# Kernel tuning notes

Measured on AMD Instinct MI355X. Metric: run time of the kernel, lower is better.

## Reference

```python
import jax, jax.numpy as jnp
import numpy as np

DIM = 768
NUM_HEADS = 12
HEAD_DIM = DIM // NUM_HEADS
SCALE = HEAD_DIM ** -0.5


def setup_inputs() -> dict:
    key = jax.random.key(0)
    k1, k2, k3, k4, k5 = jax.random.split(key, 5)
    B, N, C = 4, 2048, DIM
    x = jax.random.normal(k1, (B, N, C), dtype=jnp.float32)
    xpos = jax.random.randint(k2, (B, N), 0, 2048, dtype=jnp.int32)
    # torch Linear weights: qkv (no bias), proj (with bias)
    lim_qkv = (1.0 / C) ** 0.5
    w_qkv = jax.random.uniform(k3, (3 * C, C), minval=-lim_qkv, maxval=lim_qkv, dtype=jnp.float32)
    w_proj = jax.random.uniform(k4, (C, C), minval=-lim_qkv, maxval=lim_qkv, dtype=jnp.float32)
    b_proj = jax.random.uniform(k5, (C,), minval=-lim_qkv, maxval=lim_qkv, dtype=jnp.float32)
    return {"x": x, "xpos": xpos, "w_qkv": w_qkv, "w_proj": w_proj, "b_proj": b_proj}


def reference(x, xpos, w_qkv, w_proj, b_proj):
    B, N, C = x.shape
    H, Dh = NUM_HEADS, HEAD_DIM
    # fused QKV projection: [B,N,3C] -> [B,N,3,H,Dh] -> [B,H,3,N,Dh]
    qkv = (x @ w_qkv.T).reshape(B, N, 3, H, Dh).transpose(0, 3, 2, 1, 4)
    q, k, v = qkv[:, :, 0], qkv[:, :, 1], qkv[:, :, 2]
    # rope is None -> xpos unused
    # naive attention: materialize full [B,H,N,N] scores (matches pytorch_naive)
    scores = jnp.einsum('bhqd,bhkd->bhqk', q, k) * SCALE
    attn = jax.nn.softmax(scores, axis=-1)
    out = jnp.einsum('bhqk,bhkd->bhqd', attn, v)  # [B,H,N,Dh]
    out = out.transpose(0, 2, 1, 3).reshape(B, N, C)
    return out @ w_proj.T + b_proj
```

## Files before the change

### kernel.cpp

```cpp
#include <hip/hip_runtime.h>
#include <math.h>

typedef __bf16 bf16;
typedef __attribute__((ext_vector_type(4))) __bf16 bf16x4;
typedef __attribute__((ext_vector_type(8))) __bf16 bf16x8;
typedef __attribute__((ext_vector_type(4))) float f32x4;
typedef __attribute__((ext_vector_type(4))) unsigned int u32x4;

#define AS1 __attribute__((address_space(1)))
#define AS3 __attribute__((address_space(3)))

__device__ __forceinline__ void gload16(const void* g, void* l) {
  __builtin_amdgcn_global_load_lds((const AS1 void*)g, (AS3 void*)l, 16, 0, 0);
}

__device__ __forceinline__ unsigned int pack2bf(float lo, float hi) {
  union { unsigned int u; __bf16 h[2]; } w;
  w.h[0] = (bf16)lo; w.h[1] = (bf16)hi;
  return w.u;
}

#define DIM 768
#define NH  12
#define HD  64
#define B_  4
#define N_  2048
#define M_  (B_*N_)
#define BH_ (B_*NH)

__global__ void convert_all(const float4* __restrict__ x,
                            const float4* __restrict__ wq,
                            const float4* __restrict__ wp,
                            bf16x4* __restrict__ xb,
                            bf16x4* __restrict__ wqb,
                            bf16x4* __restrict__ wpb) {
  const int nx = M_*DIM/4, nq = 3*DIM*DIM/4, np = DIM*DIM/4;
  const int total = nx + nq + np;
  for (int i = blockIdx.x*blockDim.x + threadIdx.x; i < total;
       i += gridDim.x*blockDim.x) {
    float4 v; bf16x4* dst;
    if (i < nx)           { v = x[i];         dst = xb  + i;         }
    else if (i < nx + nq) { v = wq[i-nx];     dst = wqb + (i-nx);    }
    else                  { v = wp[i-nx-nq];  dst = wpb + (i-nx-nq); }
    bf16x4 o = { (bf16)v.x, (bf16)v.y, (bf16)v.z, (bf16)v.w };
    *dst = o;
  }
}

template<int EPI>
__global__ __launch_bounds__(256)
void gemm_bt(const bf16* __restrict__ A, const bf16* __restrict__ B,
             bf16* __restrict__ qv, bf16* __restrict__ kv_, bf16* __restrict__ vt,
             const float* __restrict__ bprj, float* __restrict__ out) {
  constexpr int K = DIM;
  __shared__ __align__(16) bf16 As[128*32];
  __shared__ __align__(16) bf16 Bs[128*32];
  const int tid = threadIdx.x;
  const int wave = tid >> 6, lane = tid & 63;
  const int l15 = lane & 15, lg = lane >> 4;
  const int wr = wave >> 1, wc = wave & 1;
  const int m0 = blockIdx.y * 128, n0 = blockIdx.x * 128;

  f32x4 acc[4][4] = {};
  const int pbase = wave*2048 + lane*16;

  for (int kb = 0; kb < K; kb += 32) {
    __syncthreads();
#pragma unroll
    for (int i = 0; i < 2; i++) {
      int p = pbase + i*1024;
      int row = p >> 6, cb = p & 63;
      gload16((const char*)A + ((size_t)(m0+row)*K + kb)*2 + cb, (char*)As + p);
      gload16((const char*)B + ((size_t)(n0+row)*K + kb)*2 + cb, (char*)Bs + p);
    }
    __syncthreads();
    bf16x8 af[4], bfr[4];
#pragma unroll
    for (int f = 0; f < 4; f++) {
      af[f]  = *(const bf16x8*)(As + (wr*64 + f*16 + l15)*32 + lg*8);
      bfr[f] = *(const bf16x8*)(Bs + (wc*64 + f*16 + l15)*32 + lg*8);
    }
#pragma unroll
    for (int fm = 0; fm < 4; fm++)
#pragma unroll
      for (int fn = 0; fn < 4; fn++)
        acc[fm][fn] = __builtin_amdgcn_mfma_f32_16x16x32_bf16(af[fm], bfr[fn],
                                                              acc[fm][fn], 0, 0, 0);
  }

  if (EPI == 0) {
    const int c0 = n0 + wc*64;
    const int t = c0 / DIM;
    const int hcol = (c0 % DIM) >> 6;
#pragma unroll
    for (int fm = 0; fm < 4; fm++) {
      const int gm0 = m0 + wr*64 + fm*16 + (lg<<2);
      const int b = gm0 >> 11, nn0 = gm0 & 2047;
      const size_t bh = (size_t)b*NH + hcol;
#pragma unroll
      for (int fn = 0; fn < 4; fn++) {
        const int d = fn*16 + l15;
        if (t == 0) {
#pragma unroll
          for (int r = 0; r < 4; r++)
            qv[(bh*N_ + nn0 + r)*HD + d] = (bf16)(acc[fm][fn][r] * 0.125f);
        } else if (t == 1) {
#pragma unroll
          for (int r = 0; r < 4; r++)
            kv_[(bh*N_ + nn0 + r)*HD + d] = (bf16)acc[fm][fn][r];
        } else {
          bf16x4 pk = { (bf16)acc[fm][fn][0], (bf16)acc[fm][fn][1],
                        (bf16)acc[fm][fn][2], (bf16)acc[fm][fn][3] };
          *(bf16x4*)(vt + (bh*HD + d)*N_ + nn0) = pk;
        }
      }
    }
  } else {
#pragma unroll
    for (int fn = 0; fn < 4; fn++) {
      const int c = n0 + wc*64 + fn*16 + l15;
      const float bias = bprj[c];
#pragma unroll
      for (int fm = 0; fm < 4; fm++) {
        const int gm0 = m0 + wr*64 + fm*16 + (lg<<2);
#pragma unroll
        for (int r = 0; r < 4; r++)
          out[(size_t)(gm0 + r)*DIM + c] = acc[fm][fn][r] + bias;
      }
    }
  }
}

__global__ __launch_bounds__(256)
void attn_fwd(const bf16* __restrict__ Q, const bf16* __restrict__ Kb,
              const bf16* __restrict__ Vt, bf16* __restrict__ AO) {
  __shared__ __align__(16) bf16 Ks[2][64*64];
  __shared__ __align__(16) bf16 Vs[2][64*64];
  const int tid = threadIdx.x;
  const int wave = tid >> 6, lane = tid & 63;
  const int l15 = lane & 15, lg = lane >> 4;
  const int bh = blockIdx.y;
  const int b = bh / NH, h = bh % NH;
  const int q0 = blockIdx.x*128 + wave*32;

  const bf16* Qbase = Q + (size_t)bh*N_*HD;
  bf16x8 qf[2][2];
#pragma unroll
  for (int fq = 0; fq < 2; fq++)
#pragma unroll
    for (int ks = 0; ks < 2; ks++)
      qf[fq][ks] = *(const bf16x8*)(Qbase + (size_t)(q0 + fq*16 + l15)*HD + ks*32 + lg*8);

  f32x4 Ot[2][4] = {};
  float m_[2] = { -INFINITY, -INFINITY };
  float l_[2] = { 0.f, 0.f };

  const char* Kg = (const char*)(Kb + (size_t)bh*N_*HD);
  const char* Vg = (const char*)(Vt + (size_t)bh*HD*N_);
  const int pbase = wave*2048 + lane*16;
  const bool lower = (lane < 32);
  const bool q03 = (lg == 0) || (lg == 3);

#define STAGE(buf, kv)                                                      \
  {                                                                         \
    _Pragma("unroll")                                                       \
    for (int i = 0; i < 2; i++) {                                           \
      int p = pbase + i*1024;                                               \
      int r = p >> 7, cbp = p & 127;                                        \
      int cb = cbp ^ ((r & 7) << 4);                                        \
      gload16(Kg + (size_t)((kv) + r)*128 + cb, (char*)Ks[buf] + p);        \
      gload16(Vg + (size_t)r*(N_*2) + (kv)*2 + cb, (char*)Vs[buf] + p);     \
    }                                                                       \
  }

  STAGE(0, 0);

  for (int t = 0; t < N_/64; ++t) {
    __syncthreads();
    if (t + 1 < N_/64) STAGE((t+1)&1, (t+1)*64);
    const char* Kc = (const char*)Ks[t&1];
    const char* Vc = (const char*)Vs[t&1];

    f32x4 s[2][4] = {};
#pragma unroll
    for (int ks = 0; ks < 2; ks++) {
      bf16x8 kf[4];
#pragma unroll
      for (int fk = 0; fk < 4; fk++) {
        int r = fk*16 + l15;
        int cb = (ks*64 + lg*16) ^ ((r & 7) << 4);
        kf[fk] = *(const bf16x8*)(Kc + r*128 + cb);
      }
#pragma unroll
      for (int fq = 0; fq < 2; fq++)
#pragma unroll
        for (int fk = 0; fk < 4; fk++)
          s[fq][fk] = __builtin_amdgcn_mfma_f32_16x16x32_bf16(kf[fk], qf[fq][ks],
                                                              s[fq][fk], 0, 0, 0);
    }

    unsigned int paw[2][2][4];
#pragma unroll
    for (int fq = 0; fq < 2; fq++) {
      float mx = s[fq][0][0];
#pragma unroll
      for (int fk = 0; fk < 4; fk++)
#pragma unroll
        for (int r = 0; r < 4; r++) mx = fmaxf(mx, s[fq][fk][r]);
      mx = fmaxf(mx, __shfl_xor(mx, 16));
      mx = fmaxf(mx, __shfl_xor(mx, 32));
      if (!__all(mx - m_[fq] <= 6.0f)) {
        float mn = fmaxf(m_[fq], mx);
        float c = __expf(m_[fq] - mn);
        m_[fq] = mn; l_[fq] *= c;
#pragma unroll
        for (int fd = 0; fd < 4; fd++) Ot[fq][fd] *= c;
      }
      float pe[4][4]; float rs = 0.f;
#pragma unroll
      for (int fk = 0; fk < 4; fk++)
#pragma unroll
        for (int r = 0; r < 4; r++) {
          pe[fk][r] = __expf(s[fq][fk][r] - m_[fq]);
          rs += pe[fk][r];
        }
      rs += __shfl_xor(rs, 16);
      rs += __shfl_xor(rs, 32);
      l_[fq] += rs;

      unsigned int pk[4][2];
#pragma unroll
      for (int fk = 0; fk < 4; fk++)
#pragma unroll
        for (int rp = 0; rp < 2; rp++)
          pk[fk][rp] = pack2bf(pe[fk][2*rp], pe[fk][2*rp+1]);

      unsigned int Eo[2][2], Er[2][2], rB[2][2];
#pragma unroll
      for (int fh = 0; fh < 2; fh++)
#pragma unroll
        for (int rp = 0; rp < 2; rp++) {
          unsigned int vA = lower ? pk[2*fh+1][rp] : pk[2*fh][rp];
          Er[fh][rp] = __shfl_xor((int)vA, 32);
          Eo[fh][rp] = lower ? pk[2*fh][rp] : pk[2*fh+1][rp];
        }
#pragma unroll
      for (int fh = 0; fh < 2; fh++)
#pragma unroll
        for (int rp = 0; rp < 2; rp++) {
          unsigned int vB = q03 ? Er[fh][rp] : Eo[fh][rp];
          rB[fh][rp] = __shfl_xor((int)vB, 16);
        }
#pragma unroll
      for (int ks = 0; ks < 2; ks++) {
#pragma unroll
        for (int rp = 0; rp < 2; rp++) {
          paw[fq][ks][rp] = (lg == 0) ? Eo[ks][rp] :
                            (lg == 1) ? rB[ks][rp] :
                            (lg == 2) ? Er[ks][rp] : rB[ks][rp];
          paw[fq][ks][2+rp] = (lg == 0) ? rB[ks][rp] :
                              (lg == 1) ? Er[ks][rp] :
                              (lg == 2) ? rB[ks][rp] : Eo[ks][rp];
        }
      }
    }

#pragma unroll
    for (int ks = 0; ks < 2; ks++) {
      bf16x8 vb[4];
#pragma unroll
      for (int fd = 0; fd < 4; fd++) {
        int r = fd*16 + l15;
        int cb = (ks*64 + lg*16) ^ ((r & 7) << 4);
        vb[fd] = *(const bf16x8*)(Vc + r*128 + cb);
      }
#pragma unroll
      for (int fq = 0; fq < 2; fq++) {
        u32x4 tw = { paw[fq][ks][0], paw[fq][ks][1], paw[fq][ks][2], paw[fq][ks][3] };
        bf16x8 pa = __builtin_bit_cast(bf16x8, tw);
#pragma unroll
        for (int fd = 0; fd < 4; fd++)
          Ot[fq][fd] = __builtin_amdgcn_mfma_f32_16x16x32_bf16(vb[fd], pa,
                                                               Ot[fq][fd], 0, 0, 0);
      }
    }
  }

#pragma unroll
  for (int fq = 0; fq < 2; fq++) {
    const float inv = 1.f / l_[fq];
    const int qrow = q0 + fq*16 + l15;
#pragma unroll
    for (int fd = 0; fd < 4; fd++) {
      bf16x4 pk4 = { (bf16)(Ot[fq][fd][0]*inv), (bf16)(Ot[fq][fd][1]*inv),
                     (bf16)(Ot[fq][fd][2]*inv), (bf16)(Ot[fq][fd][3]*inv) };
      *(bf16x4*)(AO + ((size_t)b*N_ + qrow)*DIM + h*HD + fd*16 + lg*4) = pk4;
    }
  }
#undef STAGE
}

extern "C" void kernel_launch(void* const* d_in, const int* in_sizes, int n_in,
                              void* d_out, int out_size, void* d_ws, size_t ws_size,
                              hipStream_t stream) {
  const float* x     = (const float*)d_in[0];
  const float* wqkv  = (const float*)d_in[2];
  const float* wproj = (const float*)d_in[3];
  const float* bproj = (const float*)d_in[4];
  float* out = (float*)d_out;

  char* ws = (char*)d_ws;
  bf16* xb    = (bf16*)ws;  ws += (size_t)M_*DIM*2;
  bf16* wqkvb = (bf16*)ws;  ws += (size_t)3*DIM*DIM*2;
  bf16* wprojb= (bf16*)ws;  ws += (size_t)DIM*DIM*2;
  bf16* qb    = (bf16*)ws;  ws += (size_t)BH_*N_*HD*2;
  bf16* kb    = (bf16*)ws;  ws += (size_t)BH_*N_*HD*2;
  bf16* vtb   = (bf16*)ws;  ws += (size_t)BH_*HD*N_*2;
  bf16* aob   = (bf16*)ws;  ws += (size_t)M_*DIM*2;

  convert_all<<<dim3(2048), dim3(256), 0, stream>>>(
      (const float4*)x, (const float4*)wqkv, (const float4*)wproj,
      (bf16x4*)xb, (bf16x4*)wqkvb, (bf16x4*)wprojb);

  gemm_bt<0><<<dim3(3*DIM/128, M_/128), dim3(256), 0, stream>>>(
      xb, wqkvb, qb, kb, vtb, nullptr, nullptr);

  attn_fwd<<<dim3(N_/128, BH_), dim3(256), 0, stream>>>(qb, kb, vtb, aob);

  gemm_bt<1><<<dim3(DIM/128, M_/128), dim3(256), 0, stream>>>(
      aob, wprojb, nullptr, nullptr, nullptr, bproj, out);
}
```

Measured before the change: 267.2 us.

## Halve attention query tile per block and switch softmax to exp2 with folded log2e

Each attention block now handles 64 queries (16 per wave) instead of 128, doubling the grid so more blocks are available to fill the GPU, at the cost of loading each K/V tile twice as often per query. The Q scale now folds in log2(e) so the softmax can use exp2f instead of __expf. The lazy-rescale threshold is raised to 8 in log2 units, and the row max uses a tree reduction. Per-wave MFMA work per K/V tile halves, which lowers register pressure but reduces the reuse of each shared-memory load.

```diff
diff --git a/kernel.cpp b/kernel.cpp
--- a/kernel.cpp
+++ b/kernel.cpp
@@ -27,6 +27,8 @@
 #define N_  2048
 #define M_  (B_*N_)
 #define BH_ (B_*NH)
+
+#define QSCALE 0.1803368801111244f
 
 __global__ void convert_all(const float4* __restrict__ x,
                             const float4* __restrict__ wq,
@@ -103,7 +105,7 @@
         if (t == 0) {
 #pragma unroll
           for (int r = 0; r < 4; r++)
-            qv[(bh*N_ + nn0 + r)*HD + d] = (bf16)(acc[fm][fn][r] * 0.125f);
+            qv[(bh*N_ + nn0 + r)*HD + d] = (bf16)(acc[fm][fn][r] * QSCALE);
         } else if (t == 1) {
 #pragma unroll
           for (int r = 0; r < 4; r++)
@@ -141,19 +143,16 @@
   const int l15 = lane & 15, lg = lane >> 4;
   const int bh = blockIdx.y;
   const int b = bh / NH, h = bh % NH;
-  const int q0 = blockIdx.x*128 + wave*32;
+  const int q0 = blockIdx.x*64 + wave*16;
 
   const bf16* Qbase = Q + (size_t)bh*N_*HD;
-  bf16x8 qf[2][2];
-#pragma unroll
-  for (int fq = 0; fq < 2; fq++)
-#pragma unroll
-    for (int ks = 0; ks < 2; ks++)
-      qf[fq][ks] = *(const bf16x8*)(Qbase + (size_t)(q0 + fq*16 + l15)*HD + ks*32 + lg*8);
-
-  f32x4 Ot[2][4] = {};
-  float m_[2] = { -INFINITY, -INFINITY };
-  float l_[2] = { 0.f, 0.f };
+  bf16x8 qf[2];
+#pragma unroll
+  for (int ks = 0; ks < 2; ks++)
+    qf[ks] = *(const bf16x8*)(Qbase + (size_t)(q0 + l15)*HD + ks*32 + lg*8);
+
+  f32x4 Ot[4] = {};
+  float m_ = -INFINITY, l_ = 0.f;
 
   const char* Kg = (const char*)(Kb + (size_t)bh*N_*HD);
   const char* Vg = (const char*)(Vt + (size_t)bh*HD*N_);
@@ -181,7 +180,7 @@
     const char* Kc = (const char*)Ks[t&1];
     const char* Vc = (const char*)Vs[t&1];
 
-    f32x4 s[2][4] = {};
+    f32x4 s[4] = {};
 #pragma unroll
     for (int ks = 0; ks < 2; ks++) {
       bf16x8 kf[4];
@@ -192,78 +191,75 @@
         kf[fk] = *(const bf16x8*)(Kc + r*128 + cb);
       }
 #pragma unroll
-      for (int fq = 0; fq < 2; fq++)
-#pragma unroll
-        for (int fk = 0; fk < 4; fk++)
-          s[fq][fk] = __builtin_amdgcn_mfma_f32_16x16x32_bf16(kf[fk], qf[fq][ks],
-                                                              s[fq][fk], 0, 0, 0);
-    }
-
-    unsigned int paw[2][2][4];
-#pragma unroll
-    for (int fq = 0; fq < 2; fq++) {
-      float mx = s[fq][0][0];
-#pragma unroll
       for (int fk = 0; fk < 4; fk++)
-#pragma unroll
-        for (int r = 0; r < 4; r++) mx = fmaxf(mx, s[fq][fk][r]);
-      mx = fmaxf(mx, __shfl_xor(mx, 16));
-      mx = fmaxf(mx, __shfl_xor(mx, 32));
-      if (!__all(mx - m_[fq] <= 6.0f)) {
-        float mn = fmaxf(m_[fq], mx);
-        float c = __expf(m_[fq] - mn);
-        m_[fq] = mn; l_[fq] *= c;
-#pragma unroll
-        for (int fd = 0; fd < 4; fd++) Ot[fq][fd] *= c;
-      }
-      float pe[4][4]; float rs = 0.f;
-#pragma unroll
-      for (int fk = 0; fk < 4; fk++)
-#pragma unroll
-        for (int r = 0; r < 4; r++) {
-          pe[fk][r] = __expf(s[fq][fk][r] - m_[fq]);
-          rs += pe[fk][r];
-        }
-      rs += __shfl_xor(rs, 16);
-      rs += __shfl_xor(rs, 32);
-      l_[fq] += rs;
-
-      unsigned int pk[4][2];
-#pragma unroll
-      for (int fk = 0; fk < 4; fk++)
-#pragma unroll
-        for (int rp = 0; rp < 2; rp++)
-          pk[fk][rp] = pack2bf(pe[fk][2*rp], pe[fk][2*rp+1]);
-
-      unsigned int Eo[2][2], Er[2][2], rB[2][2];
-#pragma unroll
-      for (int fh = 0; fh < 2; fh++)
-#pragma unroll
-        for (int rp = 0; rp < 2; rp++) {
-          unsigned int vA = lower ? pk[2*fh+1][rp] : pk[2*fh][rp];
-          Er[fh][rp] = __shfl_xor((int)vA, 32);
-          Eo[fh][rp] = lower ? pk[2*fh][rp] : pk[2*fh+1][rp];
-        }
-#pragma unroll
-      for (int fh = 0; fh < 2; fh++)
-#pragma unroll
-        for (int rp = 0; rp < 2; rp++) {
-          unsigned int vB = q03 ? Er[fh][rp] : Eo[fh][rp];
-          rB[fh][rp] = __shfl_xor((int)vB, 16);
-        }
-#pragma unroll
-      for (int ks = 0; ks < 2; ks++) {
-#pragma unroll
-        for (int rp = 0; rp < 2; rp++) {
-          paw[fq][ks][rp] = (lg == 0) ? Eo[ks][rp] :
-                            (lg == 1) ? rB[ks][rp] :
-                            (lg == 2) ? Er[ks][rp] : rB[ks][rp];
-          paw[fq][ks][2+rp] = (lg == 0) ? rB[ks][rp] :
-                              (lg == 1) ? Er[ks][rp] :
-                              (lg == 2) ? rB[ks][rp] : Eo[ks][rp];
-        }
-      }
-    }
+        s[fk] = __builtin_amdgcn_mfma_f32_16x16x32_bf16(kf[fk], qf[ks],
+                                                        s[fk], 0, 0, 0);
+    }
+
+    f32x4 m01, m23, m4;
+#pragma unroll
+    for (int r = 0; r < 4; r++) {
+      m01[r] = fmaxf(s[0][r], s[1][r]);
+      m23[r] = fmaxf(s[2][r], s[3][r]);
+      m4[r]  = fmaxf(m01[r], m23[r]);
+    }
+    float mx = fmaxf(fmaxf(m4[0], m4[1]), fmaxf(m4[2], m4[3]));
+    mx = fmaxf(mx, __shfl_xor(mx, 16));
+    mx = fmaxf(mx, __shfl_xor(mx, 32));
+    if (!__all(mx - m_ <= 8.0f)) {
+      float mn = fmaxf(m_, mx);
+      float c = exp2f(m_ - mn);
+      m_ = mn; l_ *= c;
+#pragma unroll
+      for (int fd = 0; fd < 4; fd++) Ot[fd] *= c;
+    }
+    float pe[4][4]; float rs = 0.f;
+#pragma unroll
+    for (int fk = 0; fk < 4; fk++)
+#pragma unroll
+      for (int r = 0; r < 4; r++) {
+        pe[fk][r] = exp2f(s[fk][r] - m_);
+        rs += pe[fk][r];
+      }
+    rs += __shfl_xor(rs, 16);
+    rs += __shfl_xor(rs, 32);
+    l_ += rs;
+
+    unsigned int pk[4][2];
+#pragma unroll
+    for (int fk = 0; fk < 4; fk++)
+#pragma unroll
+      for (int rp = 0; rp < 2; rp++)
+        pk[fk][rp] = pack2bf(pe[fk][2*rp], pe[fk][2*rp+1]);
+
+    unsigned int Eo[2][2], Er[2][2], rB[2][2];
+#pragma unroll
+    for (int fh = 0; fh < 2; fh++)
+#pragma unroll
+      for (int rp = 0; rp < 2; rp++) {
+        unsigned int vA = lower ? pk[2*fh+1][rp] : pk[2*fh][rp];
+        Er[fh][rp] = __shfl_xor((int)vA, 32);
+        Eo[fh][rp] = lower ? pk[2*fh][rp] : pk[2*fh+1][rp];
+      }
+#pragma unroll
+    for (int fh = 0; fh < 2; fh++)
+#pragma unroll
+      for (int rp = 0; rp < 2; rp++) {
+        unsigned int vB = q03 ? Er[fh][rp] : Eo[fh][rp];
+        rB[fh][rp] = __shfl_xor((int)vB, 16);
+      }
+    unsigned int paw[2][4];
+#pragma unroll
+    for (int ks = 0; ks < 2; ks++)
+#pragma unroll
+      for (int rp = 0; rp < 2; rp++) {
+        paw[ks][rp]   = (lg == 0) ? Eo[ks][rp] :
+                        (lg == 1) ? rB[ks][rp] :
+                        (lg == 2) ? Er[ks][rp] : rB[ks][rp];
+        paw[ks][2+rp] = (lg == 0) ? rB[ks][rp] :
+                        (lg == 1) ? Er[ks][rp] :
+                        (lg == 2) ? rB[ks][rp] : Eo[ks][rp];
+      }
 
 #pragma unroll
     for (int ks = 0; ks < 2; ks++) {
@@ -274,28 +270,22 @@
         int cb = (ks*64 + lg*16) ^ ((r & 7) << 4);
         vb[fd] = *(const bf16x8*)(Vc + r*128 + cb);
       }
-#pragma unroll
-      for (int fq = 0; fq < 2; fq++) {
-        u32x4 tw = { paw[fq][ks][0], paw[fq][ks][1], paw[fq][ks][2], paw[fq][ks][3] };
-        bf16x8 pa = __builtin_bit_cast(bf16x8, tw);
-#pragma unroll
-        for (int fd = 0; fd < 4; fd++)
-          Ot[fq][fd] = __builtin_amdgcn_mfma_f32_16x16x32_bf16(vb[fd], pa,
-                                                               Ot[fq][fd], 0, 0, 0);
-      }
-    }
-  }
-
-#pragma unroll
-  for (int fq = 0; fq < 2; fq++) {
-    const float inv = 1.f / l_[fq];
-    const int qrow = q0 + fq*16 + l15;
-#pragma unroll
-    for (int fd = 0; fd < 4; fd++) {
-      bf16x4 pk4 = { (bf16)(Ot[fq][fd][0]*inv), (bf16)(Ot[fq][fd][1]*inv),
-                     (bf16)(Ot[fq][fd][2]*inv), (bf16)(Ot[fq][fd][3]*inv) };
-      *(bf16x4*)(AO + ((size_t)b*N_ + qrow)*DIM + h*HD + fd*16 + lg*4) = pk4;
-    }
+      u32x4 tw = { paw[ks][0], paw[ks][1], paw[ks][2], paw[ks][3] };
+      bf16x8 pa = __builtin_bit_cast(bf16x8, tw);
+#pragma unroll
+      for (int fd = 0; fd < 4; fd++)
+        Ot[fd] = __builtin_amdgcn_mfma_f32_16x16x32_bf16(vb[fd], pa,
+                                                         Ot[fd], 0, 0, 0);
+    }
+  }
+
+  const float inv = 1.f / l_;
+  const int qrow = q0 + l15;
+#pragma unroll
+  for (int fd = 0; fd < 4; fd++) {
+    bf16x4 pk4 = { (bf16)(Ot[fd][0]*inv), (bf16)(Ot[fd][1]*inv),
+                   (bf16)(Ot[fd][2]*inv), (bf16)(Ot[fd][3]*inv) };
+    *(bf16x4*)(AO + ((size_t)b*N_ + qrow)*DIM + h*HD + fd*16 + lg*4) = pk4;
   }
 #undef STAGE
 }
@@ -325,7 +315,7 @@
   gemm_bt<0><<<dim3(3*DIM/128, M_/128), dim3(256), 0, stream>>>(
       xb, wqkvb, qb, kb, vtb, nullptr, nullptr);
 
-  attn_fwd<<<dim3(N_/128, BH_), dim3(256), 0, stream>>>(qb, kb, vtb, aob);
+  attn_fwd<<<dim3(N_/64, BH_), dim3(256), 0, stream>>>(qb, kb, vtb, aob);
 
   gemm_bt<1><<<dim3(DIM/128, M_/128), dim3(256), 0, stream>>>(
       aob, wprojb, nullptr, nullptr, nullptr, bproj, out);
```

Measured after the change: 294.6 us. +10.3%, slower.

## Split attention KV range across two blocks with a separate combine kernel

Applied to the files above, without the earlier changes.

Splits each attention block's key/value range into two halves on a third grid dimension. Each half writes unnormalised fp32 partial outputs plus running max and sum, and a new combine kernel merges them into the bf16 attention output. The Q scale now folds in log2(e), so the softmax can use exp2f; the rescale threshold is raised and the max reduction becomes a tree. This adds parallelism and shortens each block's loop, at the cost of extra fp32 partial traffic and an additional kernel launch.

```diff
diff --git a/kernel.cpp b/kernel.cpp
--- a/kernel.cpp
+++ b/kernel.cpp
@@ -27,6 +27,10 @@
 #define N_  2048
 #define M_  (B_*N_)
 #define BH_ (B_*NH)
+#define NSPLIT 2
+#define KVLEN (N_/NSPLIT)
+
+#define QSCALE 0.1803368801111244f
 
 __global__ void convert_all(const float4* __restrict__ x,
                             const float4* __restrict__ wq,
@@ -103,7 +107,7 @@
         if (t == 0) {
 #pragma unroll
           for (int r = 0; r < 4; r++)
-            qv[(bh*N_ + nn0 + r)*HD + d] = (bf16)(acc[fm][fn][r] * 0.125f);
+            qv[(bh*N_ + nn0 + r)*HD + d] = (bf16)(acc[fm][fn][r] * QSCALE);
         } else if (t == 1) {
 #pragma unroll
           for (int r = 0; r < 4; r++)
@@ -133,14 +137,15 @@
 
 __global__ __launch_bounds__(256)
 void attn_fwd(const bf16* __restrict__ Q, const bf16* __restrict__ Kb,
-              const bf16* __restrict__ Vt, bf16* __restrict__ AO) {
+              const bf16* __restrict__ Vt,
+              float* __restrict__ Opart, float* __restrict__ Mlpart) {
   __shared__ __align__(16) bf16 Ks[2][64*64];
   __shared__ __align__(16) bf16 Vs[2][64*64];
   const int tid = threadIdx.x;
   const int wave = tid >> 6, lane = tid & 63;
   const int l15 = lane & 15, lg = lane >> 4;
   const int bh = blockIdx.y;
-  const int b = bh / NH, h = bh % NH;
+  const int spl = blockIdx.z;
   const int q0 = blockIdx.x*128 + wave*32;
 
   const bf16* Qbase = Q + (size_t)bh*N_*HD;
@@ -155,8 +160,8 @@
   float m_[2] = { -INFINITY, -INFINITY };
   float l_[2] = { 0.f, 0.f };
 
-  const char* Kg = (const char*)(Kb + (size_t)bh*N_*HD);
-  const char* Vg = (const char*)(Vt + (size_t)bh*HD*N_);
+  const char* Kg = (const char*)(Kb + (size_t)bh*N_*HD) + (size_t)spl*KVLEN*128;
+  const char* Vg = (const char*)(Vt + (size_t)bh*HD*N_) + (size_t)spl*KVLEN*2;
   const int pbase = wave*2048 + lane*16;
   const bool lower = (lane < 32);
   const bool q03 = (lg == 0) || (lg == 3);
@@ -175,9 +180,9 @@
 
   STAGE(0, 0);
 
-  for (int t = 0; t < N_/64; ++t) {
+  for (int t = 0; t < KVLEN/64; ++t) {
     __syncthreads();
-    if (t + 1 < N_/64) STAGE((t+1)&1, (t+1)*64);
+    if (t + 1 < KVLEN/64) STAGE((t+1)&1, (t+1)*64);
     const char* Kc = (const char*)Ks[t&1];
     const char* Vc = (const char*)Vs[t&1];
 
@@ -202,16 +207,19 @@
     unsigned int paw[2][2][4];
 #pragma unroll
     for (int fq = 0; fq < 2; fq++) {
-      float mx = s[fq][0][0];
-#pragma unroll
-      for (int fk = 0; fk < 4; fk++)
-#pragma unroll
-        for (int r = 0; r < 4; r++) mx = fmaxf(mx, s[fq][fk][r]);
+      float mx = fmaxf(fmaxf(fmaxf(s[fq][0][0], s[fq][0][1]),
+                             fmaxf(s[fq][0][2], s[fq][0][3])),
+                       fmaxf(fmaxf(s[fq][1][0], s[fq][1][1]),
+                             fmaxf(s[fq][1][2], s[fq][1][3])));
+      mx = fmaxf(mx, fmaxf(fmaxf(fmaxf(s[fq][2][0], s[fq][2][1]),
+                                 fmaxf(s[fq][2][2], s[fq][2][3])),
+                           fmaxf(fmaxf(s[fq][3][0], s[fq][3][1]),
+                                 fmaxf(s[fq][3][2], s[fq][3][3]))));
       mx = fmaxf(mx, __shfl_xor(mx, 16));
       mx = fmaxf(mx, __shfl_xor(mx, 32));
-      if (!__all(mx - m_[fq] <= 6.0f)) {
+      if (!__all(mx - m_[fq] <= 8.0f)) {
         float mn = fmaxf(m_[fq], mx);
-        float c = __expf(m_[fq] - mn);
+        float c = exp2f(m_[fq] - mn);
         m_[fq] = mn; l_[fq] *= c;
 #pragma unroll
         for (int fd = 0; fd < 4; fd++) Ot[fq][fd] *= c;
@@ -221,7 +229,7 @@
       for (int fk = 0; fk < 4; fk++)
 #pragma unroll
         for (int r = 0; r < 4; r++) {
-          pe[fk][r] = __expf(s[fq][fk][r] - m_[fq]);
+          pe[fk][r] = exp2f(s[fq][fk][r] - m_[fq]);
           rs += pe[fk][r];
         }
       rs += __shfl_xor(rs, 16);
@@ -286,18 +294,41 @@
     }
   }
 
+  float* Ob  = Opart  + ((size_t)spl*BH_ + bh)*N_*HD;
+  float* Mlb = Mlpart + ((size_t)spl*BH_ + bh)*N_*2;
 #pragma unroll
   for (int fq = 0; fq < 2; fq++) {
-    const float inv = 1.f / l_[fq];
     const int qrow = q0 + fq*16 + l15;
-#pragma unroll
-    for (int fd = 0; fd < 4; fd++) {
-      bf16x4 pk4 = { (bf16)(Ot[fq][fd][0]*inv), (bf16)(Ot[fq][fd][1]*inv),
-                     (bf16)(Ot[fq][fd][2]*inv), (bf16)(Ot[fq][fd][3]*inv) };
-      *(bf16x4*)(AO + ((size_t)b*N_ + qrow)*DIM + h*HD + fd*16 + lg*4) = pk4;
-    }
+    if (lg == 0) {
+      Mlb[(size_t)qrow*2]     = m_[fq];
+      Mlb[(size_t)qrow*2 + 1] = l_[fq];
+    }
+#pragma unroll
+    for (int fd = 0; fd < 4; fd++)
+      *(f32x4*)(Ob + (size_t)qrow*HD + fd*16 + lg*4) = Ot[fq][fd];
   }
 #undef STAGE
+}
+
+__global__ __launch_bounds__(256)
+void attn_combine(const float* __restrict__ Op, const float* __restrict__ Ml,
+                  bf16* __restrict__ AO) {
+  const int g = blockIdx.x*256 + threadIdx.x;
+  const int dq = g & 15;
+  const int row = g >> 4;
+  const int bh = row >> 11, n = row & 2047;
+  const float m0 = Ml[(size_t)row*2],                 l0 = Ml[(size_t)row*2 + 1];
+  const float m1 = Ml[((size_t)BH_*N_ + row)*2],      l1 = Ml[((size_t)BH_*N_ + row)*2 + 1];
+  const float mM = fmaxf(m0, m1);
+  const float w0 = exp2f(m0 - mM), w1 = exp2f(m1 - mM);
+  const float inv = 1.f / (l0*w0 + l1*w1);
+  f32x4 o0 = *(const f32x4*)(Op + (size_t)row*HD + dq*4);
+  f32x4 o1 = *(const f32x4*)(Op + ((size_t)BH_*N_ + row)*HD + dq*4);
+  const int b = bh / NH, hed = bh % NH;
+  bf16x4 r;
+#pragma unroll
+  for (int i = 0; i < 4; i++) r[i] = (bf16)((o0[i]*w0 + o1[i]*w1) * inv);
+  *(bf16x4*)(AO + ((size_t)b*N_ + n)*DIM + hed*HD + dq*4) = r;
 }
 
 extern "C" void kernel_launch(void* const* d_in, const int* in_sizes, int n_in,
@@ -317,6 +348,8 @@
   bf16* kb    = (bf16*)ws;  ws += (size_t)BH_*N_*HD*2;
   bf16* vtb   = (bf16*)ws;  ws += (size_t)BH_*HD*N_*2;
   bf16* aob   = (bf16*)ws;  ws += (size_t)M_*DIM*2;
+  float* opart = (float*)ws; ws += (size_t)NSPLIT*BH_*N_*HD*4;
+  float* mlprt = (float*)ws; ws += (size_t)NSPLIT*BH_*N_*2*4;
 
   convert_all<<<dim3(2048), dim3(256), 0, stream>>>(
       (const float4*)x, (const float4*)wqkv, (const float4*)wproj,
@@ -325,7 +358,11 @@
   gemm_bt<0><<<dim3(3*DIM/128, M_/128), dim3(256), 0, stream>>>(
       xb, wqkvb, qb, kb, vtb, nullptr, nullptr);
 
-  attn_fwd<<<dim3(N_/128, BH_), dim3(256), 0, stream>>>(qb, kb, vtb, aob);
+  attn_fwd<<<dim3(N_/128, BH_, NSPLIT), dim3(256), 0, stream>>>(
+      qb, kb, vtb, opart, mlprt);
+
+  attn_combine<<<dim3(BH_*N_*16/256), dim3(256), 0, stream>>>(
+      opart, mlprt, aob);
 
   gemm_bt<1><<<dim3(DIM/128, M_/128), dim3(256), 0, stream>>>(
       aob, wprojb, nullptr, nullptr, nullptr, bproj, out);
```

Measured after the change: 325.5 us. 21.8% more time.
